# Kernel optimization log

Measured on AMD Instinct MI355X. Metric: run time of the kernel, lower is better.

## Reference

```python
import jax, jax.numpy as jnp
import numpy as np
import math

DIM_Q = 512; DIM_K = 512; DIM_V = 512; H = 8; EPS = 1e-5

def _layernorm(x, g, b):
    mu = jnp.mean(x, axis=-1, keepdims=True)
    var = jnp.mean((x - mu) ** 2, axis=-1, keepdims=True)
    return (x - mu) * jax.lax.rsqrt(var + EPS) * g + b

def setup_inputs() -> dict:
    key = jax.random.key(0)
    ks = jax.random.split(key, 12)
    B, NQ, NK = 8, 1024, 1024
    s = 0.02
    return {
        "Q": jax.random.normal(ks[0], (B, NQ, DIM_Q), jnp.float32),
        "K": jax.random.normal(ks[1], (B, NK, DIM_K), jnp.float32),
        "attention_mask": jax.random.randint(ks[2], (B, NK), 0, 2, jnp.int32),
        "Wq": jax.random.normal(ks[3], (DIM_Q, DIM_V), jnp.float32) * s,
        "bq": jnp.zeros((DIM_V,), jnp.float32),
        "Wk": jax.random.normal(ks[4], (DIM_K, DIM_V), jnp.float32) * s,
        "bk": jnp.zeros((DIM_V,), jnp.float32),
        "Wv": jax.random.normal(ks[5], (DIM_K, DIM_V), jnp.float32) * s,
        "bv": jnp.zeros((DIM_V,), jnp.float32),
        "Wo": jax.random.normal(ks[6], (DIM_V, DIM_V), jnp.float32) * s,
        "bo": jnp.zeros((DIM_V,), jnp.float32),
        "g0": jnp.ones((DIM_V,), jnp.float32),
        "b0": jnp.zeros((DIM_V,), jnp.float32),
        "g1": jnp.ones((DIM_V,), jnp.float32),
        "b1": jnp.zeros((DIM_V,), jnp.float32),
    }

def reference(Q, K, attention_mask, Wq, bq, Wk, bk, Wv, bv, Wo, bo, g0, b0, g1, b1):
    B, NQ, _ = Q.shape
    NK = K.shape[1]
    dh = DIM_V // H
    q = (Q @ Wq + bq).reshape(B, NQ, H, dh).transpose(0, 2, 1, 3)  # (B,H,NQ,dh)
    k = (K @ Wk + bk).reshape(B, NK, H, dh).transpose(0, 2, 1, 3)
    v = (K @ Wv + bv).reshape(B, NK, H, dh).transpose(0, 2, 1, 3)
    # NOTE: original scales by sqrt(dim_V), not sqrt(head_dim)
    scores = jnp.einsum("bhqd,bhkd->bhqk", q, k) / math.sqrt(DIM_V)
    scores = jnp.where(attention_mask[:, None, None, :] == 0, -10000.0, scores)
    A = jax.nn.softmax(scores, axis=-1)
    o = q + jnp.einsum("bhqk,bhkd->bhqd", A, v)  # residual before output proj
    O = o.transpose(0, 2, 1, 3).reshape(B, NQ, DIM_V)
    O = _layernorm(O, g0, b0)
    O = O + jax.nn.relu(O @ Wo + bo)
    O = _layernorm(O, g1, b1)
    return O
```

## Files before the change

kernel.cpp:

```cpp
#include <hip/hip_runtime.h>
#include <hip/hip_bf16.h>

typedef __attribute__((ext_vector_type(8))) short short8;
typedef __attribute__((ext_vector_type(4))) short short4v;
typedef __attribute__((ext_vector_type(4))) float float4v;
typedef __attribute__((ext_vector_type(4))) unsigned uint4v;

#define LDK 72
#define LDV 136
#define SCALE2 0.06376540791556074f
#define MBIAS2 -14426.950408889634f
#define PCLAMP 12.0f

__device__ inline unsigned short f2b(float f) {
    return __builtin_bit_cast(unsigned short, __float2bfloat16(f));
}
__device__ inline float b2f(unsigned short s) {
    return __uint_as_float(((unsigned)s) << 16);
}
__device__ inline unsigned pk2(float lo, float hi) {
    return (unsigned)f2b(lo) | ((unsigned)f2b(hi) << 16);
}
__device__ __forceinline__ void gld16(const unsigned short* g, unsigned short* l) {
    __builtin_amdgcn_global_load_lds(
        (const __attribute__((address_space(1))) void*)g,
        (__attribute__((address_space(3))) void*)l, 16, 0, 0);
}

__global__ void cast_bf16_kernel(const float* __restrict__ in,
                                 unsigned short* __restrict__ out, int n) {
    int i = (blockIdx.x * blockDim.x + threadIdx.x) * 8;
    if (i < n) {
        float4v a = *(const float4v*)(in + i);
        float4v b = *(const float4v*)(in + i + 4);
        uint4v o = {pk2(a[0], a[1]), pk2(a[2], a[3]), pk2(b[0], b[1]), pk2(b[2], b[3])};
        *(uint4v*)(out + i) = o;
    }
}

__global__ void transpose_w_kernel(const float* __restrict__ W0, const float* __restrict__ W1,
                                   const float* __restrict__ W2, const float* __restrict__ W3,
                                   unsigned short* __restrict__ out) {
    const float* W = (blockIdx.z == 0) ? W0 : (blockIdx.z == 1) ? W1
                   : (blockIdx.z == 2) ? W2 : W3;
    unsigned short* o = out + (size_t)blockIdx.z * 512 * 512;
    __shared__ float tile[32][33];
    int k0 = blockIdx.x * 32, n0 = blockIdx.y * 32;
    int tx = threadIdx.x & 31, ty = threadIdx.x >> 5;
    for (int r = ty; r < 32; r += 8) tile[r][tx] = W[(size_t)(k0 + r) * 512 + n0 + tx];
    __syncthreads();
    for (int r = ty; r < 32; r += 8) o[(size_t)(n0 + r) * 512 + k0 + tx] = f2b(tile[tx][r]);
}

__global__ __launch_bounds__(256) void gemm_kernel(
    const unsigned short* __restrict__ Qb, const unsigned short* __restrict__ Kb,
    const unsigned short* __restrict__ hb, const unsigned short* __restrict__ WT,
    const float* __restrict__ bq, const float* __restrict__ bk,
    const float* __restrict__ bv, const float* __restrict__ bo,
    unsigned short* __restrict__ qo, unsigned short* __restrict__ ko,
    unsigned short* __restrict__ vTo, unsigned short* __restrict__ to_,
    int zbase) {
    int z = zbase + blockIdx.z;
    const unsigned short* A = (z == 0) ? Qb : (z == 3) ? hb : Kb;
    const unsigned short* BT = WT + (size_t)z * 512 * 512;
    const float* bias = (z == 0) ? bq : (z == 1) ? bk : (z == 2) ? bv : bo;

    __shared__ unsigned short As[128 * 64];
    __shared__ unsigned short Bs[128 * 64];

    int tid = threadIdx.x;
    int lane = tid & 63, wave = tid >> 6;
    int wr = wave >> 1, wc = wave & 1;
    int l15 = lane & 15, lg = lane >> 4;
    int row0 = blockIdx.x * 128, col0 = blockIdx.y * 128;

    float4v acc[4][4];
#pragma unroll
    for (int m = 0; m < 4; m++)
#pragma unroll
        for (int n = 0; n < 4; n++) acc[m][n] = (float4v){0.f, 0.f, 0.f, 0.f};

    int srow = wave * 32 + (lane >> 3);
    int gch = (lane & 7) ^ (srow & 7);
    const unsigned short* gA = A + (size_t)(row0 + srow) * 512 + gch * 8;
    const unsigned short* gB = BT + (size_t)(col0 + srow) * 512 + gch * 8;
    unsigned short* lA = As + wave * 2048;
    unsigned short* lB = Bs + wave * 2048;
    int sw = l15 & 7;

    for (int k0 = 0; k0 < 512; k0 += 64) {
        __syncthreads();
#pragma unroll
        for (int c = 0; c < 4; c++) {
            gld16(gA + (size_t)c * 4096 + k0, lA + c * 512);
            gld16(gB + (size_t)c * 4096 + k0, lB + c * 512);
        }
        __syncthreads();
#pragma unroll
        for (int kk = 0; kk < 2; kk++) {
            int ck = ((kk * 4 + lg) ^ sw) * 8;
            short8 af[4], bf[4];
#pragma unroll
            for (int m = 0; m < 4; m++)
                af[m] = *(const short8*)(As + (wr * 64 + m * 16 + l15) * 64 + ck);
#pragma unroll
            for (int n = 0; n < 4; n++)
                bf[n] = *(const short8*)(Bs + (wc * 64 + n * 16 + l15) * 64 + ck);
#pragma unroll
            for (int m = 0; m < 4; m++)
#pragma unroll
                for (int n = 0; n < 4; n++)
                    acc[m][n] = __builtin_amdgcn_mfma_f32_16x16x32_bf16(af[m], bf[n], acc[m][n], 0, 0, 0);
        }
    }

#pragma unroll
    for (int n = 0; n < 4; n++) {
        int col = col0 + wc * 64 + n * 16 + l15;
        float bias_v = bias[col];
#pragma unroll
        for (int m = 0; m < 4; m++) {
            int rowb = row0 + wr * 64 + m * 16 + lg * 4;
            float4v v = acc[m][n];
            if (z == 2) {
                int b = rowb >> 10, tq = rowb & 1023;
                int h = col >> 6, d = col & 63;
                short4v st;
#pragma unroll
                for (int r = 0; r < 4; r++) st[r] = (short)f2b(v[r] + bias_v);
                *(short4v*)(vTo + ((((size_t)b * 8 + h) * 64 + d) << 10) + tq) = st;
            } else if (z == 3) {
#pragma unroll
                for (int r = 0; r < 4; r++) {
                    size_t idx = (size_t)(rowb + r) * 512 + col;
                    float x = v[r] + bias_v;
                    x = x > 0.f ? x : 0.f;
                    to_[idx] = f2b(x + b2f(hb[idx]));
                }
            } else {
                unsigned short* o = (z == 0) ? qo : ko;
#pragma unroll
                for (int r = 0; r < 4; r++)
                    o[(size_t)(rowb + r) * 512 + col] = f2b(v[r] + bias_v);
            }
        }
    }
}

__global__ __launch_bounds__(256) void attn_kernel(
    const unsigned short* __restrict__ qb, const unsigned short* __restrict__ kb,
    const unsigned short* __restrict__ vT, const int* __restrict__ mask,
    unsigned short* __restrict__ ob) {
    __shared__ unsigned short Ks[128 * LDK];
    __shared__ unsigned short Vs[64 * LDV];
    __shared__ float mbias[128];

    int tid = threadIdx.x;
    int lane = tid & 63, wave = tid >> 6;
    int l15 = lane & 15, lg = lane >> 4;
    int bh = blockIdx.y;
    int b = bh >> 3, h = bh & 7;
    int qrow0 = b * 1024 + blockIdx.x * 64 + wave * 16;

    short8 qf[2];
#pragma unroll
    for (int kk = 0; kk < 2; kk++)
        qf[kk] = *(const short8*)(qb + (size_t)(qrow0 + l15) * 512 + h * 64 + kk * 32 + lg * 8);

    float l_acc = 0.f;
    float4v oacc[4];
#pragma unroll
    for (int n = 0; n < 4; n++) oacc[n] = (float4v){0.f, 0.f, 0.f, 0.f};

    int stok = tid >> 1, skoff = (tid & 1) * 32;
    int prow = (stok & 0x63) | ((stok & 4) << 2) | ((stok & 0x18) >> 1);
    int svd = tid >> 2, svoff = (tid & 3) * 32;

    for (int jt = 0; jt < 8; jt++) {
        __syncthreads();
        {
            const unsigned short* kg =
                kb + (size_t)(b * 1024 + jt * 128 + stok) * 512 + h * 64 + skoff;
            *(short8*)(Ks + prow * LDK + skoff)      = *(const short8*)kg;
            *(short8*)(Ks + prow * LDK + skoff + 8)  = *(const short8*)(kg + 8);
            *(short8*)(Ks + prow * LDK + skoff + 16) = *(const short8*)(kg + 16);
            *(short8*)(Ks + prow * LDK + skoff + 24) = *(const short8*)(kg + 24);
            const unsigned short* vg =
                vT + (((size_t)bh * 64 + svd) << 10) + jt * 128 + svoff;
            *(short8*)(Vs + svd * LDV + svoff)      = *(const short8*)vg;
            *(short8*)(Vs + svd * LDV + svoff + 8)  = *(const short8*)(vg + 8);
            *(short8*)(Vs + svd * LDV + svoff + 16) = *(const short8*)(vg + 16);
            *(short8*)(Vs + svd * LDV + svoff + 24) = *(const short8*)(vg + 24);
            if (tid < 128) mbias[tid] = mask[b * 1024 + jt * 128 + tid] ? 0.f : MBIAS2;
        }
        __syncthreads();

        float p[8][4];
#pragma unroll
        for (int jf = 0; jf < 8; jf++) {
            short8 kf0 = *(const short8*)(Ks + (jf * 16 + l15) * LDK + lg * 8);
            short8 kf1 = *(const short8*)(Ks + (jf * 16 + l15) * LDK + 32 + lg * 8);
            float4v t = (float4v){0.f, 0.f, 0.f, 0.f};
            t = __builtin_amdgcn_mfma_f32_16x16x32_bf16(kf0, qf[0], t, 0, 0, 0);
            t = __builtin_amdgcn_mfma_f32_16x16x32_bf16(kf1, qf[1], t, 0, 0, 0);
#pragma unroll
            for (int r = 0; r < 4; r++) p[jf][r] = t[r];
        }
#pragma unroll
        for (int jf = 0; jf < 8; jf++)
#pragma unroll
            for (int r = 0; r < 4; r++) {
                float val = fminf(fmaf(p[jf][r], SCALE2,
                                       mbias[32 * (jf >> 1) + 8 * lg + 4 * (jf & 1) + r]),
                                  PCLAMP);
                float e = exp2f(val);
                p[jf][r] = e;
                l_acc += e;
            }

        short8 pb[4];
#pragma unroll
        for (int ks = 0; ks < 4; ks++) {
            uint4v w = {pk2(p[2 * ks][0], p[2 * ks][1]), pk2(p[2 * ks][2], p[2 * ks][3]),
                        pk2(p[2 * ks + 1][0], p[2 * ks + 1][1]),
                        pk2(p[2 * ks + 1][2], p[2 * ks + 1][3])};
            pb[ks] = __builtin_bit_cast(short8, w);
        }

#pragma unroll
        for (int n = 0; n < 4; n++)
#pragma unroll
            for (int ks = 0; ks < 4; ks++) {
                short8 vf = *(const short8*)(Vs + (n * 16 + l15) * LDV + ks * 32 + lg * 8);
                oacc[n] = __builtin_amdgcn_mfma_f32_16x16x32_bf16(vf, pb[ks], oacc[n], 0, 0, 0);
            }
    }

    l_acc += __shfl_xor(l_acc, 16);
    l_acc += __shfl_xor(l_acc, 32);
    float inv = 1.f / l_acc;
#pragma unroll
    for (int n = 0; n < 4; n++) {
        size_t base = (size_t)(qrow0 + l15) * 512 + h * 64 + n * 16 + lg * 4;
        short4v qr = *(const short4v*)(qb + base);
        short4v st;
#pragma unroll
        for (int r = 0; r < 4; r++)
            st[r] = (short)f2b(b2f((unsigned short)qr[r]) + oacc[n][r] * inv);
        *(short4v*)(ob + base) = st;
    }
}

__global__ void ln_kernel_bf16(const unsigned short* __restrict__ in,
                               const float* __restrict__ g, const float* __restrict__ bb,
                               unsigned short* __restrict__ out) {
    int row = blockIdx.x, lane = threadIdx.x;
    short8 v = *(const short8*)(in + (size_t)row * 512 + lane * 8);
    float x[8], s = 0.f, s2 = 0.f;
#pragma unroll
    for (int j = 0; j < 8; j++) {
        x[j] = b2f((unsigned short)v[j]);
        s += x[j];
        s2 += x[j] * x[j];
    }
#pragma unroll
    for (int off = 1; off < 64; off <<= 1) {
        s += __shfl_xor(s, off);
        s2 += __shfl_xor(s2, off);
    }
    float mu = s * (1.f / 512.f);
    float var = s2 * (1.f / 512.f) - mu * mu;
    float rs = rsqrtf(var + 1e-5f);
#pragma unroll
    for (int j = 0; j < 8; j++) {
        int c = lane * 8 + j;
        out[(size_t)row * 512 + c] = f2b((x[j] - mu) * rs * g[c] + bb[c]);
    }
}

__global__ void ln_kernel_f32(const unsigned short* __restrict__ in,
                              const float* __restrict__ g, const float* __restrict__ bb,
                              float* __restrict__ out) {
    int row = blockIdx.x, lane = threadIdx.x;
    short8 v = *(const short8*)(in + (size_t)row * 512 + lane * 8);
    float x[8], s = 0.f, s2 = 0.f;
#pragma unroll
    for (int j = 0; j < 8; j++) {
        x[j] = b2f((unsigned short)v[j]);
        s += x[j];
        s2 += x[j] * x[j];
    }
#pragma unroll
    for (int off = 1; off < 64; off <<= 1) {
        s += __shfl_xor(s, off);
        s2 += __shfl_xor(s2, off);
    }
    float mu = s * (1.f / 512.f);
    float var = s2 * (1.f / 512.f) - mu * mu;
    float rs = rsqrtf(var + 1e-5f);
#pragma unroll
    for (int j = 0; j < 8; j++) {
        int c = lane * 8 + j;
        out[(size_t)row * 512 + c] = (x[j] - mu) * rs * g[c] + bb[c];
    }
}

extern "C" void kernel_launch(void* const* d_in, const int* in_sizes, int n_in,
                              void* d_out, int out_size, void* d_ws, size_t ws_size,
                              hipStream_t stream) {
    const float* Q = (const float*)d_in[0];
    const float* K = (const float*)d_in[1];
    const int* mask = (const int*)d_in[2];
    const float* Wq = (const float*)d_in[3];
    const float* bq = (const float*)d_in[4];
    const float* Wk = (const float*)d_in[5];
    const float* bk = (const float*)d_in[6];
    const float* Wv = (const float*)d_in[7];
    const float* bv = (const float*)d_in[8];
    const float* Wo = (const float*)d_in[9];
    const float* bo = (const float*)d_in[10];
    const float* g0 = (const float*)d_in[11];
    const float* b0 = (const float*)d_in[12];
    const float* g1 = (const float*)d_in[13];
    const float* b1 = (const float*)d_in[14];
    float* out = (float*)d_out;

    const size_t N = 8192ull * 512;
    unsigned short* w16 = (unsigned short*)d_ws;
    unsigned short* Qb = w16;
    unsigned short* Kb = Qb + N;
    unsigned short* WT = Kb + N;
    unsigned short* qb = WT + 4ull * 512 * 512;
    unsigned short* kb = qb + N;
    unsigned short* vTb = kb + N;
    unsigned short* obuf = vTb + N;
    unsigned short* hbuf = obuf + N;
    unsigned short* tbuf = hbuf + N;

    cast_bf16_kernel<<<2048, 256, 0, stream>>>(Q, Qb, (int)N);
    cast_bf16_kernel<<<2048, 256, 0, stream>>>(K, Kb, (int)N);
    transpose_w_kernel<<<dim3(16, 16, 4), 256, 0, stream>>>(Wq, Wk, Wv, Wo, WT);
    gemm_kernel<<<dim3(64, 4, 3), 256, 0, stream>>>(Qb, Kb, hbuf, WT, bq, bk, bv, bo,
                                                    qb, kb, vTb, tbuf, 0);
    attn_kernel<<<dim3(16, 64), 256, 0, stream>>>(qb, kb, vTb, mask, obuf);
    ln_kernel_bf16<<<8192, 64, 0, stream>>>(obuf, g0, b0, hbuf);
    gemm_kernel<<<dim3(64, 4, 1), 256, 0, stream>>>(Qb, Kb, hbuf, WT, bq, bk, bv, bo,
                                                    qb, kb, vTb, tbuf, 3);
    ln_kernel_f32<<<8192, 64, 0, stream>>>(tbuf, g1, b1, out);
}
```

Baseline: 204.3 us.

## Double-buffer GEMM and attention tiles, coalesce GEMM epilogue through LDS

The GEMM kernel now double-buffers its A/B LDS tiles, issuing async global-to-LDS loads for the next K slice while the current one is computed, so one barrier per iteration is removed. Its q/k/t epilogue stages results in LDS and writes 16-byte coalesced rows, including a vectorized residual add for the z==3 path. The attention kernel moves to 64-key tiles with register prefetch and double-buffered K/V/mask LDS, overlapping global loads with MFMA work. The costs are more LDS per block in the GEMM, which may lower occupancy, and twice as many attention iterations.

```diff
diff --git a/kernel.cpp b/kernel.cpp
--- a/kernel.cpp
+++ b/kernel.cpp
@@ -7,10 +7,10 @@
 typedef __attribute__((ext_vector_type(4))) unsigned uint4v;
 
 #define LDK 72
-#define LDV 136
 #define SCALE2 0.06376540791556074f
 #define MBIAS2 -14426.950408889634f
 #define PCLAMP 12.0f
+#define EPS 76
 
 __device__ inline unsigned short f2b(float f) {
     return __builtin_bit_cast(unsigned short, __float2bfloat16(f));
@@ -65,8 +65,7 @@
     const unsigned short* BT = WT + (size_t)z * 512 * 512;
     const float* bias = (z == 0) ? bq : (z == 1) ? bk : (z == 2) ? bv : bo;
 
-    __shared__ unsigned short As[128 * 64];
-    __shared__ unsigned short Bs[128 * 64];
+    __shared__ unsigned short SM[4][8192];
 
     int tid = threadIdx.x;
     int lane = tid & 63, wave = tid >> 6;
@@ -84,18 +83,21 @@
     int gch = (lane & 7) ^ (srow & 7);
     const unsigned short* gA = A + (size_t)(row0 + srow) * 512 + gch * 8;
     const unsigned short* gB = BT + (size_t)(col0 + srow) * 512 + gch * 8;
-    unsigned short* lA = As + wave * 2048;
-    unsigned short* lB = Bs + wave * 2048;
     int sw = l15 & 7;
 
-    for (int k0 = 0; k0 < 512; k0 += 64) {
-        __syncthreads();
+    auto STAGE = [&](int bi, int t) {
+        unsigned short* lA = SM[bi * 2] + wave * 2048;
+        unsigned short* lB = SM[bi * 2 + 1] + wave * 2048;
+        int k0 = t * 64;
 #pragma unroll
         for (int c = 0; c < 4; c++) {
             gld16(gA + (size_t)c * 4096 + k0, lA + c * 512);
             gld16(gB + (size_t)c * 4096 + k0, lB + c * 512);
         }
-        __syncthreads();
+    };
+    auto COMPUTE = [&](int bi) {
+        const unsigned short* As = SM[bi * 2];
+        const unsigned short* Bs = SM[bi * 2 + 1];
 #pragma unroll
         for (int kk = 0; kk < 2; kk++) {
             int ck = ((kk * 4 + lg) ^ sw) * 8;
@@ -112,36 +114,69 @@
                 for (int n = 0; n < 4; n++)
                     acc[m][n] = __builtin_amdgcn_mfma_f32_16x16x32_bf16(af[m], bf[n], acc[m][n], 0, 0, 0);
         }
-    }
-
-#pragma unroll
-    for (int n = 0; n < 4; n++) {
-        int col = col0 + wc * 64 + n * 16 + l15;
-        float bias_v = bias[col];
-#pragma unroll
-        for (int m = 0; m < 4; m++) {
-            int rowb = row0 + wr * 64 + m * 16 + lg * 4;
-            float4v v = acc[m][n];
-            if (z == 2) {
+    };
+
+    STAGE(0, 0);
+    __syncthreads();
+    int buf = 0;
+    for (int t = 0; t < 7; t++) {
+        STAGE(buf ^ 1, t + 1);
+        COMPUTE(buf);
+        __syncthreads();
+        buf ^= 1;
+    }
+    COMPUTE(buf);
+
+    if (z == 2) {
+#pragma unroll
+        for (int n = 0; n < 4; n++) {
+            int col = col0 + wc * 64 + n * 16 + l15;
+            float bias_v = bias[col];
+            int h = col >> 6, d = col & 63;
+#pragma unroll
+            for (int m = 0; m < 4; m++) {
+                int rowb = row0 + wr * 64 + m * 16 + lg * 4;
                 int b = rowb >> 10, tq = rowb & 1023;
-                int h = col >> 6, d = col & 63;
+                float4v v = acc[m][n];
                 short4v st;
 #pragma unroll
                 for (int r = 0; r < 4; r++) st[r] = (short)f2b(v[r] + bias_v);
                 *(short4v*)(vTo + ((((size_t)b * 8 + h) * 64 + d) << 10) + tq) = st;
-            } else if (z == 3) {
+            }
+        }
+    } else {
+        __syncthreads();
+        unsigned short* ep = &SM[0][0] + wave * (64 * EPS);
+#pragma unroll
+        for (int n = 0; n < 4; n++) {
+            float bias_v = bias[col0 + wc * 64 + n * 16 + l15];
+#pragma unroll
+            for (int m = 0; m < 4; m++) {
+                float4v v = acc[m][n];
 #pragma unroll
                 for (int r = 0; r < 4; r++) {
-                    size_t idx = (size_t)(rowb + r) * 512 + col;
                     float x = v[r] + bias_v;
-                    x = x > 0.f ? x : 0.f;
-                    to_[idx] = f2b(x + b2f(hb[idx]));
+                    if (z == 3) x = x > 0.f ? x : 0.f;
+                    ep[(m * 16 + lg * 4 + r) * EPS + n * 16 + l15] = f2b(x);
                 }
+            }
+        }
+        int lr = lane >> 3, lc = lane & 7;
+        unsigned short* o = (z == 0) ? qo : (z == 1) ? ko : to_;
+#pragma unroll
+        for (int p = 0; p < 8; p++) {
+            int row_l = p * 8 + lr;
+            short8 vv = *(const short8*)(ep + row_l * EPS + lc * 8);
+            size_t gidx = (size_t)(row0 + wr * 64 + row_l) * 512 + col0 + wc * 64 + lc * 8;
+            if (z == 3) {
+                short8 hv = *(const short8*)(hb + gidx);
+                short8 o8;
+#pragma unroll
+                for (int j = 0; j < 8; j++)
+                    o8[j] = (short)f2b(b2f((unsigned short)vv[j]) + b2f((unsigned short)hv[j]));
+                *(short8*)(o + gidx) = o8;
             } else {
-                unsigned short* o = (z == 0) ? qo : ko;
-#pragma unroll
-                for (int r = 0; r < 4; r++)
-                    o[(size_t)(rowb + r) * 512 + col] = f2b(v[r] + bias_v);
+                *(short8*)(o + gidx) = vv;
             }
         }
     }
@@ -151,9 +186,9 @@
     const unsigned short* __restrict__ qb, const unsigned short* __restrict__ kb,
     const unsigned short* __restrict__ vT, const int* __restrict__ mask,
     unsigned short* __restrict__ ob) {
-    __shared__ unsigned short Ks[128 * LDK];
-    __shared__ unsigned short Vs[64 * LDV];
-    __shared__ float mbias[128];
+    __shared__ unsigned short Ks[2][64 * LDK];
+    __shared__ unsigned short Vs[2][64 * LDK];
+    __shared__ float mb[2][64];
 
     int tid = threadIdx.x;
     int lane = tid & 63, wave = tid >> 6;
@@ -172,68 +207,82 @@
 #pragma unroll
     for (int n = 0; n < 4; n++) oacc[n] = (float4v){0.f, 0.f, 0.f, 0.f};
 
-    int stok = tid >> 1, skoff = (tid & 1) * 32;
-    int prow = (stok & 0x63) | ((stok & 4) << 2) | ((stok & 0x18) >> 1);
-    int svd = tid >> 2, svoff = (tid & 3) * 32;
-
-    for (int jt = 0; jt < 8; jt++) {
-        __syncthreads();
-        {
-            const unsigned short* kg =
-                kb + (size_t)(b * 1024 + jt * 128 + stok) * 512 + h * 64 + skoff;
-            *(short8*)(Ks + prow * LDK + skoff)      = *(const short8*)kg;
-            *(short8*)(Ks + prow * LDK + skoff + 8)  = *(const short8*)(kg + 8);
-            *(short8*)(Ks + prow * LDK + skoff + 16) = *(const short8*)(kg + 16);
-            *(short8*)(Ks + prow * LDK + skoff + 24) = *(const short8*)(kg + 24);
-            const unsigned short* vg =
-                vT + (((size_t)bh * 64 + svd) << 10) + jt * 128 + svoff;
-            *(short8*)(Vs + svd * LDV + svoff)      = *(const short8*)vg;
-            *(short8*)(Vs + svd * LDV + svoff + 8)  = *(const short8*)(vg + 8);
-            *(short8*)(Vs + svd * LDV + svoff + 16) = *(const short8*)(vg + 16);
-            *(short8*)(Vs + svd * LDV + svoff + 24) = *(const short8*)(vg + 24);
-            if (tid < 128) mbias[tid] = mask[b * 1024 + jt * 128 + tid] ? 0.f : MBIAS2;
-        }
-        __syncthreads();
-
-        float p[8][4];
-#pragma unroll
-        for (int jf = 0; jf < 8; jf++) {
-            short8 kf0 = *(const short8*)(Ks + (jf * 16 + l15) * LDK + lg * 8);
-            short8 kf1 = *(const short8*)(Ks + (jf * 16 + l15) * LDK + 32 + lg * 8);
-            float4v t = (float4v){0.f, 0.f, 0.f, 0.f};
-            t = __builtin_amdgcn_mfma_f32_16x16x32_bf16(kf0, qf[0], t, 0, 0, 0);
-            t = __builtin_amdgcn_mfma_f32_16x16x32_bf16(kf1, qf[1], t, 0, 0, 0);
-#pragma unroll
-            for (int r = 0; r < 4; r++) p[jf][r] = t[r];
-        }
-#pragma unroll
-        for (int jf = 0; jf < 8; jf++)
+    int srow = tid >> 2, soff = (tid & 2) * 16;
+    int shalf = (tid & 1) * 16;
+    int koff = soff + shalf;
+    int prow = (srow & 0x23) | ((srow & 4) << 2) | ((srow & 0x18) >> 1);
+
+    short8 kreg[2], vreg[2];
+    int mreg = 0;
+    auto LOADR = [&](int t) {
+        const unsigned short* kg = kb + (size_t)(b * 1024 + t * 64 + srow) * 512 + h * 64 + koff;
+        kreg[0] = *(const short8*)kg;
+        kreg[1] = *(const short8*)(kg + 8);
+        const unsigned short* vg = vT + (((size_t)bh * 64 + srow) << 10) + t * 64 + koff;
+        vreg[0] = *(const short8*)vg;
+        vreg[1] = *(const short8*)(vg + 8);
+        if (tid < 64) mreg = mask[b * 1024 + t * 64 + tid];
+    };
+    auto WLDS = [&](int bi) {
+        *(short8*)(Ks[bi] + prow * LDK + koff) = kreg[0];
+        *(short8*)(Ks[bi] + prow * LDK + koff + 8) = kreg[1];
+        *(short8*)(Vs[bi] + srow * LDK + koff) = vreg[0];
+        *(short8*)(Vs[bi] + srow * LDK + koff + 8) = vreg[1];
+        if (tid < 64) mb[bi][tid] = mreg ? 0.f : MBIAS2;
+    };
+
+    LOADR(0);
+    WLDS(0);
+    __syncthreads();
+    int buf = 0;
+    for (int t = 0; t < 16; t++) {
+        if (t < 15) LOADR(t + 1);
+
+        const unsigned short* Kc = Ks[buf];
+        const unsigned short* Vc = Vs[buf];
+        float p[4][4];
+#pragma unroll
+        for (int jf = 0; jf < 4; jf++) {
+            short8 kf0 = *(const short8*)(Kc + (jf * 16 + l15) * LDK + lg * 8);
+            short8 kf1 = *(const short8*)(Kc + (jf * 16 + l15) * LDK + 32 + lg * 8);
+            float4v tt = (float4v){0.f, 0.f, 0.f, 0.f};
+            tt = __builtin_amdgcn_mfma_f32_16x16x32_bf16(kf0, qf[0], tt, 0, 0, 0);
+            tt = __builtin_amdgcn_mfma_f32_16x16x32_bf16(kf1, qf[1], tt, 0, 0, 0);
+#pragma unroll
+            for (int r = 0; r < 4; r++) p[jf][r] = tt[r];
+        }
+#pragma unroll
+        for (int jf = 0; jf < 4; jf++)
 #pragma unroll
             for (int r = 0; r < 4; r++) {
                 float val = fminf(fmaf(p[jf][r], SCALE2,
-                                       mbias[32 * (jf >> 1) + 8 * lg + 4 * (jf & 1) + r]),
+                                       mb[buf][32 * (jf >> 1) + 8 * lg + 4 * (jf & 1) + r]),
                                   PCLAMP);
                 float e = exp2f(val);
                 p[jf][r] = e;
                 l_acc += e;
             }
-
-        short8 pb[4];
-#pragma unroll
-        for (int ks = 0; ks < 4; ks++) {
+        short8 pb[2];
+#pragma unroll
+        for (int ks = 0; ks < 2; ks++) {
             uint4v w = {pk2(p[2 * ks][0], p[2 * ks][1]), pk2(p[2 * ks][2], p[2 * ks][3]),
                         pk2(p[2 * ks + 1][0], p[2 * ks + 1][1]),
                         pk2(p[2 * ks + 1][2], p[2 * ks + 1][3])};
             pb[ks] = __builtin_bit_cast(short8, w);
         }
-
 #pragma unroll
         for (int n = 0; n < 4; n++)
 #pragma unroll
-            for (int ks = 0; ks < 4; ks++) {
-                short8 vf = *(const short8*)(Vs + (n * 16 + l15) * LDV + ks * 32 + lg * 8);
+            for (int ks = 0; ks < 2; ks++) {
+                short8 vf = *(const short8*)(Vc + (n * 16 + l15) * LDK + ks * 32 + lg * 8);
                 oacc[n] = __builtin_amdgcn_mfma_f32_16x16x32_bf16(vf, pb[ks], oacc[n], 0, 0, 0);
             }
+
+        if (t < 15) {
+            WLDS(buf ^ 1);
+            __syncthreads();
+            buf ^= 1;
+        }
     }
 
     l_acc += __shfl_xor(l_acc, 16);
```

Measured after the change: 191.2 us. 6.4% less time.
